# Kernel optimization log

Measured on AMD Instinct MI355X. Metric: run time of the kernel, lower is better.

## Reference

```python
import jax, jax.numpy as jnp
import numpy as np

EPS = 1e-12  # torch F.normalize default eps


def setup_inputs() -> dict:
    key = jax.random.key(0)
    k1, k2, k3, k4 = jax.random.split(key, 4)
    B, M, D = 4, 8192, 512
    N, P = 128, 1
    x = jax.random.normal(k1, (B, M, D), dtype=jnp.float32)
    phi = jax.random.normal(k2, (D, N, P), dtype=jnp.float32) * (1.0 / D ** 0.5)
    scale = jnp.ones((1,), dtype=jnp.float32)
    W = jax.random.normal(k3, (N, D, D), dtype=jnp.float32) * (1.0 / D ** 0.5)
    b = jax.random.normal(k4, (N, D), dtype=jnp.float32) * 0.01
    return {"x": x, "phi": phi, "scale": scale, "W": W, "b": b}


def _l2norm(v, axis):
    return v / jnp.maximum(jnp.linalg.norm(v, axis=axis, keepdims=True), EPS)


def reference(x, phi, scale, W, b):
    # normalize tokens along feature dim, phi along dim axis, scale phi
    xn = _l2norm(x, axis=2)                      # [B,M,D]
    phin = scale * _l2norm(phi, axis=0)          # [D,N,P]
    logits = jnp.einsum('bmd,dnp->bmnp', xn, phin)
    B, M, N, P = logits.shape
    d = jax.nn.softmax(logits, axis=1)           # dispatch weights (over tokens)
    c = jax.nn.softmax(logits.reshape(B, M, N * P), axis=-1).reshape(B, M, N, P)  # combine (over slots)
    xs = jnp.einsum('bmd,bmnp->bnpd', xn, d)     # slot inputs [B,N,P,D]
    # per-expert Linear, batched over experts (grouped GEMM)
    ys = jnp.einsum('bnpd,nde->bnpe', xs, W) + b[None, :, None, :]
    y = jnp.einsum('bnpd,bmnp->bmd', ys, c)
    return y
```

## Files before the change

### kernel.cpp

```cpp
#include <hip/hip_runtime.h>
#include <math.h>

#define B_ 4
#define M_ 8192
#define D_ 512
#define N_ 128
#define TOK (B_ * M_)
#define MC_ 64
#define MLEN (M_ / MC_)

#define OFF_RN 0
#define OFF_CS (OFF_RN + TOK)
#define OFF_XS (OFF_CS + 512)
#define OFF_YS (OFF_XS + B_ * N_ * D_)
#define OFF_PBT (OFF_YS + B_ * N_ * D_)
#define OFF_YST (OFF_PBT + N_ * D_ / 2)
#define OFF_E (OFF_YST + B_ * D_ * N_ / 2)
#define OFF_XP (OFF_E + (size_t)TOK * N_)

typedef __attribute__((ext_vector_type(8))) short s16x8;
typedef __attribute__((ext_vector_type(4))) float f32x4;

__device__ inline short f2bf(float f) {
    union { float f; unsigned u; } v;
    v.f = f;
    unsigned r = v.u + 0x7fffu + ((v.u >> 16) & 1u);
    return (short)(r >> 16);
}

__global__ __launch_bounds__(128) void k_phinorm(const float* __restrict__ phi,
                                                 const float* __restrict__ scale,
                                                 short* __restrict__ pbt) {
    __shared__ float sred[128];
    int n = blockIdx.x, tid = threadIdx.x;
    float ss = 0.f;
    for (int d = tid; d < D_; d += 128) {
        float v = phi[d * N_ + n];
        ss += v * v;
    }
    sred[tid] = ss;
    __syncthreads();
    for (int s = 64; s > 0; s >>= 1) {
        if (tid < s) sred[tid] += sred[tid + s];
        __syncthreads();
    }
    float sc = scale[0] / fmaxf(sqrtf(sred[0]), 1e-12f);
    for (int d = tid; d < D_; d += 128) pbt[n * D_ + d] = f2bf(phi[d * N_ + n] * sc);
}

__global__ __launch_bounds__(256) void k_rn(const float* __restrict__ x,
                                            float* __restrict__ rn) {
    int token = blockIdx.x * 4 + (threadIdx.x >> 6);
    int lane = threadIdx.x & 63;
    const float4* x4 = (const float4*)x;
    float4 a = x4[(size_t)token * 128 + lane];
    float4 c = x4[(size_t)token * 128 + 64 + lane];
    float ss = a.x * a.x + a.y * a.y + a.z * a.z + a.w * a.w +
               c.x * c.x + c.y * c.y + c.z * c.z + c.w * c.w;
#pragma unroll
    for (int off = 32; off > 0; off >>= 1) ss += __shfl_down(ss, off, 64);
    if (lane == 0) rn[token] = 1.0f / fmaxf(sqrtf(ss), 1e-12f);
}

__global__ __launch_bounds__(512) void k_logits(const float* __restrict__ x,
                                                const short* __restrict__ pbt,
                                                const float* __restrict__ rn,
                                                float* __restrict__ E,
                                                float* __restrict__ colsum) {
    __shared__ short As[128 * 40];
    __shared__ short Bs[128 * 40];
    int t = threadIdx.x;
    int r0 = blockIdx.x * 128;
    int sm = t >> 2;
    int kq = (t & 3) * 8;
    float rnv = rn[r0 + sm];
    const float* xrow = &x[(size_t)(r0 + sm) * D_ + kq];
    const short* brow = &pbt[sm * D_ + kq];
    int wid = t >> 6, lane = t & 63;
    int quad = lane >> 4, l15 = lane & 15;
    int mw = (wid >> 1) * 32, nw = (wid & 1) * 64;
    f32x4 acc[2][4] = {};

    for (int k0 = 0; k0 < D_; k0 += 32) {
        float4 a0 = *(const float4*)&xrow[k0];
        float4 a1 = *(const float4*)&xrow[k0 + 4];
        s16x8 bv = *(const s16x8*)&brow[k0];
        short4 w0 = {f2bf(a0.x * rnv), f2bf(a0.y * rnv), f2bf(a0.z * rnv), f2bf(a0.w * rnv)};
        short4 w1 = {f2bf(a1.x * rnv), f2bf(a1.y * rnv), f2bf(a1.z * rnv), f2bf(a1.w * rnv)};
        *(short4*)&As[sm * 40 + kq] = w0;
        *(short4*)&As[sm * 40 + kq + 4] = w1;
        *(s16x8*)&Bs[sm * 40 + kq] = bv;
        __syncthreads();
        s16x8 af[2], bf[4];
#pragma unroll
        for (int i = 0; i < 2; i++)
            af[i] = *(const s16x8*)&As[(mw + i * 16 + l15) * 40 + quad * 8];
#pragma unroll
        for (int j = 0; j < 4; j++)
            bf[j] = *(const s16x8*)&Bs[(nw + j * 16 + l15) * 40 + quad * 8];
#pragma unroll
        for (int i = 0; i < 2; i++)
#pragma unroll
            for (int j = 0; j < 4; j++)
                acc[i][j] = __builtin_amdgcn_mfma_f32_16x16x32_bf16(af[i], bf[j], acc[i][j], 0, 0, 0);
        __syncthreads();
    }
    int bb = r0 >> 13;
#pragma unroll
    for (int j = 0; j < 4; j++) {
        int n = nw + j * 16 + l15;
        float cs = 0.f;
#pragma unroll
        for (int i = 0; i < 2; i++) {
            int mb = r0 + mw + i * 16 + quad * 4;
            f32x4 v = acc[i][j];
            float e0 = __expf(v[0]), e1 = __expf(v[1]), e2 = __expf(v[2]), e3 = __expf(v[3]);
            cs += e0 + e1 + e2 + e3;
            E[(size_t)(mb + 0) * N_ + n] = e0;
            E[(size_t)(mb + 1) * N_ + n] = e1;
            E[(size_t)(mb + 2) * N_ + n] = e2;
            E[(size_t)(mb + 3) * N_ + n] = e3;
        }
        cs += __shfl_xor(cs, 16, 64);
        cs += __shfl_xor(cs, 32, 64);
        if (lane < 16) atomicAdd(&colsum[bb * N_ + n], cs);
    }
}

__global__ __launch_bounds__(256) void k_xs(const float* __restrict__ x,
                                            const float* __restrict__ E,
                                            const float* __restrict__ rn,
                                            float* __restrict__ part) {
    __shared__ float Et[16][128];
    __shared__ float xt[16][128];
    int tid = threadIdx.x, bi = blockIdx.x;
    int dt = bi & 3, mc = (bi >> 2) & 63, b = bi >> 8;
    int d0 = dt * 128;
    int rbase = b * M_ + mc * MLEN;
    int ty = tid >> 4, tx = tid & 15;
    float acc[8][8];
#pragma unroll
    for (int i = 0; i < 8; i++)
#pragma unroll
        for (int j = 0; j < 8; j++) acc[i][j] = 0.f;

    for (int ms = 0; ms < MLEN; ms += 16) {
        int rb = rbase + ms;
        {
            int lmm = tid >> 4, lc4 = (tid & 15) * 4;
            float rr = rn[rb + lmm];
            const float* Er = &E[(size_t)(rb + lmm) * N_];
            const float* xr = &x[(size_t)(rb + lmm) * D_ + d0];
            float4 v0 = *(const float4*)&Er[lc4];
            float4 v1 = *(const float4*)&Er[64 + lc4];
            v0.x *= rr; v0.y *= rr; v0.z *= rr; v0.w *= rr;
            v1.x *= rr; v1.y *= rr; v1.z *= rr; v1.w *= rr;
            *(float4*)&Et[lmm][lc4] = v0;
            *(float4*)&Et[lmm][64 + lc4] = v1;
            *(float4*)&xt[lmm][lc4] = *(const float4*)&xr[lc4];
            *(float4*)&xt[lmm][64 + lc4] = *(const float4*)&xr[64 + lc4];
        }
        __syncthreads();
#pragma unroll
        for (int kk = 0; kk < 16; kk++) {
            float4 a0 = *(float4*)&Et[kk][ty * 4];
            float4 a1 = *(float4*)&Et[kk][64 + ty * 4];
            float4 b0 = *(float4*)&xt[kk][tx * 4];
            float4 b1 = *(float4*)&xt[kk][64 + tx * 4];
            float a8[8] = {a0.x, a0.y, a0.z, a0.w, a1.x, a1.y, a1.z, a1.w};
            float b8[8] = {b0.x, b0.y, b0.z, b0.w, b1.x, b1.y, b1.z, b1.w};
#pragma unroll
            for (int i = 0; i < 8; i++)
#pragma unroll
                for (int j = 0; j < 8; j++) acc[i][j] += a8[i] * b8[j];
        }
        __syncthreads();
    }
#pragma unroll
    for (int i = 0; i < 8; i++) {
        int n = (i < 4) ? (ty * 4 + i) : (64 + ty * 4 + (i - 4));
        size_t base = (((size_t)mc * B_ + b) * N_ + n) * D_ + d0;
        float4 v0 = {acc[i][0], acc[i][1], acc[i][2], acc[i][3]};
        float4 v1 = {acc[i][4], acc[i][5], acc[i][6], acc[i][7]};
        *(float4*)&part[base + tx * 4] = v0;
        *(float4*)&part[base + 64 + tx * 4] = v1;
    }
}

__global__ __launch_bounds__(256) void k_xsum(const float* __restrict__ part,
                                              const float* __restrict__ colsum,
                                              float* __restrict__ xs) {
    int bi = blockIdx.x;
    int tid = threadIdx.x;
    float inv = 1.0f / colsum[bi];
    size_t base = (size_t)bi * D_ + tid * 2;
    float sx = 0.f, sy = 0.f;
#pragma unroll 8
    for (int mc = 0; mc < MC_; mc++) {
        float2 v = *(const float2*)&part[(size_t)mc * (B_ * N_ * D_) + base];
        sx += v.x;
        sy += v.y;
    }
    float2 o = {sx * inv, sy * inv};
    *(float2*)&xs[base] = o;
}

__global__ __launch_bounds__(256) void k_ys(const float* __restrict__ xs,
                                            const float* __restrict__ W,
                                            const float* __restrict__ bias,
                                            float* __restrict__ ys) {
    __shared__ float xsn[B_][D_];
    int bi = blockIdx.x;
    int n = bi >> 2, eq = bi & 3;
    int tid = threadIdx.x;
    {
        int lb = tid >> 6, ld = (tid & 63) * 4;
        *(float4*)&xsn[lb][ld] = *(const float4*)&xs[((size_t)lb * N_ + n) * D_ + ld];
        *(float4*)&xsn[lb][256 + ld] =
            *(const float4*)&xs[((size_t)lb * N_ + n) * D_ + 256 + ld];
    }
    __syncthreads();
    int b = tid >> 6;
    int e = eq * 128 + (tid & 63) * 2;
    const float* Wn = W + (size_t)n * D_ * D_ + e;
    float a0 = 0.f, a1 = 0.f;
#pragma unroll 8
    for (int d = 0; d < D_; d++) {
        float2 w = *(const float2*)&Wn[(size_t)d * D_];
        float xv = xsn[b][d];
        a0 += xv * w.x;
        a1 += xv * w.y;
    }
    float2 bv = *(const float2*)&bias[n * D_ + e];
    float2 o = {a0 + bv.x, a1 + bv.y};
    *(float2*)&ys[((size_t)b * N_ + n) * D_ + e] = o;
}

__global__ __launch_bounds__(256) void k_yst(const float* __restrict__ ys,
                                             short* __restrict__ ysT) {
    __shared__ float tile[32][33];
    int bi = blockIdx.x;
    int nt = bi & 3, dt = (bi >> 2) & 15, b = bi >> 6;
    int n0 = nt * 32, d0 = dt * 32;
    int t = threadIdx.x;
    int r = t >> 3, c = (t & 7) * 4;
    float4 v = *(const float4*)&ys[((size_t)b * N_ + n0 + r) * D_ + d0 + c];
    tile[r][c] = v.x; tile[r][c + 1] = v.y; tile[r][c + 2] = v.z; tile[r][c + 3] = v.w;
    __syncthreads();
    short4 o = {f2bf(tile[c][r]), f2bf(tile[c + 1][r]), f2bf(tile[c + 2][r]),
                f2bf(tile[c + 3][r])};
    *(short4*)&ysT[((size_t)b * D_ + d0 + r) * N_ + n0 + c] = o;
}

__global__ __launch_bounds__(256) void k_combine(const float* __restrict__ E,
                                                 const short* __restrict__ ysT,
                                                 float* __restrict__ y) {
    __shared__ short As[128 * 40];
    __shared__ short Bs[128 * 40];
    __shared__ float rsA[2][128];
    __shared__ float rsinv[128];
    int t = threadIdx.x, bi = blockIdx.x;
    int dt = bi & 3, mt = bi >> 2;
    int r0 = mt * 128, d0 = dt * 128;
    int bb = r0 >> 13;
    int sm = t >> 1, nh = (t & 1) * 16;
    const float* erow = &E[(size_t)(r0 + sm) * N_ + nh];
    const short* yrow = &ysT[((size_t)bb * D_ + d0 + sm) * N_ + nh];
    int wid = t >> 6, lane = t & 63;
    int quad = lane >> 4, l15 = lane & 15;
    int mw = (wid >> 1) * 64, dw = (wid & 1) * 64;
    f32x4 acc[4][4] = {};
    float rsp = 0.f;

    for (int ks = 0; ks < 4; ks++) {
        int n0 = ks * 32;
        float4 e0 = *(const float4*)&erow[n0];
        float4 e1 = *(const float4*)&erow[n0 + 4];
        float4 e2 = *(const float4*)&erow[n0 + 8];
        float4 e3 = *(const float4*)&erow[n0 + 12];
        rsp += e0.x + e0.y + e0.z + e0.w + e1.x + e1.y + e1.z + e1.w +
               e2.x + e2.y + e2.z + e2.w + e3.x + e3.y + e3.z + e3.w;
        short4 w0 = {f2bf(e0.x), f2bf(e0.y), f2bf(e0.z), f2bf(e0.w)};
        short4 w1 = {f2bf(e1.x), f2bf(e1.y), f2bf(e1.z), f2bf(e1.w)};
        short4 w2 = {f2bf(e2.x), f2bf(e2.y), f2bf(e2.z), f2bf(e2.w)};
        short4 w3 = {f2bf(e3.x), f2bf(e3.y), f2bf(e3.z), f2bf(e3.w)};
        *(short4*)&As[sm * 40 + nh + 0] = w0;
        *(short4*)&As[sm * 40 + nh + 4] = w1;
        *(short4*)&As[sm * 40 + nh + 8] = w2;
        *(short4*)&As[sm * 40 + nh + 12] = w3;
        *(s16x8*)&Bs[sm * 40 + nh] = *(const s16x8*)&yrow[n0];
        *(s16x8*)&Bs[sm * 40 + nh + 8] = *(const s16x8*)&yrow[n0 + 8];
        __syncthreads();
        s16x8 af[4], bf[4];
#pragma unroll
        for (int i = 0; i < 4; i++)
            af[i] = *(const s16x8*)&As[(mw + i * 16 + l15) * 40 + quad * 8];
#pragma unroll
        for (int j = 0; j < 4; j++)
            bf[j] = *(const s16x8*)&Bs[(dw + j * 16 + l15) * 40 + quad * 8];
#pragma unroll
        for (int i = 0; i < 4; i++)
#pragma unroll
            for (int j = 0; j < 4; j++)
                acc[i][j] = __builtin_amdgcn_mfma_f32_16x16x32_bf16(af[i], bf[j], acc[i][j], 0, 0, 0);
        __syncthreads();
    }
    rsA[t & 1][sm] = rsp;
    __syncthreads();
    if (t < 128) rsinv[t] = 1.0f / (rsA[0][t] + rsA[1][t]);
    __syncthreads();
#pragma unroll
    for (int i = 0; i < 4; i++) {
        int mb = mw + i * 16 + quad * 4;
        float i0 = rsinv[mb], i1 = rsinv[mb + 1], i2 = rsinv[mb + 2], i3 = rsinv[mb + 3];
#pragma unroll
        for (int j = 0; j < 4; j++) {
            int d = d0 + dw + j * 16 + l15;
            f32x4 v = acc[i][j];
            y[(size_t)(r0 + mb + 0) * D_ + d] = v[0] * i0;
            y[(size_t)(r0 + mb + 1) * D_ + d] = v[1] * i1;
            y[(size_t)(r0 + mb + 2) * D_ + d] = v[2] * i2;
            y[(size_t)(r0 + mb + 3) * D_ + d] = v[3] * i3;
        }
    }
}

extern "C" void kernel_launch(void* const* d_in, const int* in_sizes, int n_in,
                              void* d_out, int out_size, void* d_ws, size_t ws_size,
                              hipStream_t stream) {
    const float* x = (const float*)d_in[0];
    const float* phi = (const float*)d_in[1];
    const float* scale = (const float*)d_in[2];
    const float* W = (const float*)d_in[3];
    const float* bias = (const float*)d_in[4];
    float* y = (float*)d_out;
    float* ws = (float*)d_ws;

    float* rn = ws + OFF_RN;
    float* colsum = ws + OFF_CS;
    float* xs = ws + OFF_XS;
    float* ysb = ws + OFF_YS;
    short* pbt = (short*)(ws + OFF_PBT);
    short* ysT = (short*)(ws + OFF_YST);
    float* E = ws + OFF_E;
    float* part = ws + OFF_XP;

    hipMemsetAsync(colsum, 0, 512 * sizeof(float), stream);

    k_phinorm<<<N_, 128, 0, stream>>>(phi, scale, pbt);
    k_rn<<<TOK / 4, 256, 0, stream>>>(x, rn);
    k_logits<<<TOK / 128, 512, 0, stream>>>(x, pbt, rn, E, colsum);
    k_xs<<<B_ * MC_ * 4, 256, 0, stream>>>(x, E, rn, part);
    k_xsum<<<B_ * N_, 256, 0, stream>>>(part, colsum, xs);
    k_ys<<<N_ * 4, 256, 0, stream>>>(xs, W, bias, ysb);
    k_yst<<<B_ * 16 * 4, 256, 0, stream>>>(ysb, ysT);
    k_combine<<<(TOK / 128) * 4, 256, 0, stream>>>(E, ysT, y);
}
```

Baseline: 374.4 us.

## Move dispatch reduction onto bf16 MFMA with pre-transposed normalized inputs

A new prep kernel normalizes x once, writing bf16 row-major and token-transposed copies, and replaces the separate row-norm kernel. The logits kernel now reads bf16 x and additionally writes a transposed bf16 copy of exp(logits). The slot-input reduction (k_xs) becomes a bf16 MFMA GEMM over tokens instead of an FP32 scalar outer-product loop, with half as many token chunks. The ys kernel writes the transposed bf16 output directly, which removes the separate transpose kernel. This trades extra workspace traffic and reduced precision in the dispatch sum for matrix-core throughput.

Result: faster. 355.5 us (-5.1%).

```diff
diff --git a/kernel.cpp b/kernel.cpp
--- a/kernel.cpp
+++ b/kernel.cpp
@@ -6,17 +6,18 @@
 #define D_ 512
 #define N_ 128
 #define TOK (B_ * M_)
-#define MC_ 64
+#define MC_ 32
 #define MLEN (M_ / MC_)
 
-#define OFF_RN 0
-#define OFF_CS (OFF_RN + TOK)
+#define OFF_CS 0
 #define OFF_XS (OFF_CS + 512)
-#define OFF_YS (OFF_XS + B_ * N_ * D_)
-#define OFF_PBT (OFF_YS + B_ * N_ * D_)
-#define OFF_YST (OFF_PBT + N_ * D_ / 2)
-#define OFF_E (OFF_YST + B_ * D_ * N_ / 2)
-#define OFF_XP (OFF_E + (size_t)TOK * N_)
+#define OFF_PBT (OFF_XS + B_ * N_ * D_)
+#define OFF_E (OFF_PBT + N_ * D_ / 2)
+#define OFF_EWT (OFF_E + (size_t)TOK * N_)
+#define OFF_XB (OFF_EWT + (size_t)N_ * TOK / 2)
+#define OFF_XBT (OFF_XB + (size_t)TOK * D_ / 2)
+#define OFF_YST (OFF_XBT + (size_t)D_ * TOK / 2)
+#define OFF_XP (OFF_YST + B_ * D_ * N_ / 2)
 
 typedef __attribute__((ext_vector_type(8))) short s16x8;
 typedef __attribute__((ext_vector_type(4))) float f32x4;
@@ -48,33 +49,69 @@
     for (int d = tid; d < D_; d += 128) pbt[n * D_ + d] = f2bf(phi[d * N_ + n] * sc);
 }
 
-__global__ __launch_bounds__(256) void k_rn(const float* __restrict__ x,
-                                            float* __restrict__ rn) {
-    int token = blockIdx.x * 4 + (threadIdx.x >> 6);
-    int lane = threadIdx.x & 63;
-    const float4* x4 = (const float4*)x;
-    float4 a = x4[(size_t)token * 128 + lane];
-    float4 c = x4[(size_t)token * 128 + 64 + lane];
-    float ss = a.x * a.x + a.y * a.y + a.z * a.z + a.w * a.w +
-               c.x * c.x + c.y * c.y + c.z * c.z + c.w * c.w;
-#pragma unroll
-    for (int off = 32; off > 0; off >>= 1) ss += __shfl_down(ss, off, 64);
-    if (lane == 0) rn[token] = 1.0f / fmaxf(sqrtf(ss), 1e-12f);
-}
-
-__global__ __launch_bounds__(512) void k_logits(const float* __restrict__ x,
+__global__ __launch_bounds__(256) void k_prep(const float* __restrict__ x,
+                                              short* __restrict__ xb,
+                                              short* __restrict__ xbt) {
+    __shared__ short T[512 * 40];
+    __shared__ float sred[32][8];
+    __shared__ float srn[32];
+    int t = threadIdx.x;
+    int m0 = blockIdx.x * 32;
+    int row = t >> 3, o8 = t & 7;
+    const float4* xr = (const float4*)&x[(size_t)(m0 + row) * D_ + o8 * 64];
+    float4 v[16];
+    float ss = 0.f;
+#pragma unroll
+    for (int i = 0; i < 16; i++) {
+        v[i] = xr[i];
+        ss += v[i].x * v[i].x + v[i].y * v[i].y + v[i].z * v[i].z + v[i].w * v[i].w;
+    }
+    sred[row][o8] = ss;
+    __syncthreads();
+    if (t < 32) {
+        float s = sred[t][0] + sred[t][1] + sred[t][2] + sred[t][3] +
+                  sred[t][4] + sred[t][5] + sred[t][6] + sred[t][7];
+        srn[t] = 1.0f / fmaxf(sqrtf(s), 1e-12f);
+    }
+    __syncthreads();
+    float rv = srn[row];
+    short* xrow = &xb[(size_t)(m0 + row) * D_ + o8 * 64];
+    int slot = (row + 8 * (o8 & 3)) & 31;
+    int dbase = o8 * 64;
+#pragma unroll
+    for (int i = 0; i < 16; i++) {
+        short4 w = {f2bf(v[i].x * rv), f2bf(v[i].y * rv), f2bf(v[i].z * rv), f2bf(v[i].w * rv)};
+        *(short4*)&xrow[i * 4] = w;
+        int d = dbase + i * 4;
+        T[(d + 0) * 40 + slot] = w.x;
+        T[(d + 1) * 40 + slot] = w.y;
+        T[(d + 2) * 40 + slot] = w.z;
+        T[(d + 3) * 40 + slot] = w.w;
+    }
+    __syncthreads();
+#pragma unroll
+    for (int p = 0; p < 8; p++) {
+        int d = p * 64 + (t >> 2);
+        int g = t & 3;
+        int sgrp = (g + ((d >> 6) & 3)) & 3;
+        s16x8 val = *(const s16x8*)&T[d * 40 + sgrp * 8];
+        *(s16x8*)&xbt[(size_t)d * TOK + m0 + g * 8] = val;
+    }
+}
+
+__global__ __launch_bounds__(512) void k_logits(const short* __restrict__ xb,
                                                 const short* __restrict__ pbt,
-                                                const float* __restrict__ rn,
                                                 float* __restrict__ E,
+                                                short* __restrict__ ewt,
                                                 float* __restrict__ colsum) {
-    __shared__ short As[128 * 40];
-    __shared__ short Bs[128 * 40];
+    __shared__ short smem[2 * 128 * 40];
+    short* As = smem;
+    short* Bs = smem + 128 * 40;
     int t = threadIdx.x;
     int r0 = blockIdx.x * 128;
     int sm = t >> 2;
     int kq = (t & 3) * 8;
-    float rnv = rn[r0 + sm];
-    const float* xrow = &x[(size_t)(r0 + sm) * D_ + kq];
+    const short* xrow = &xb[(size_t)(r0 + sm) * D_ + kq];
     const short* brow = &pbt[sm * D_ + kq];
     int wid = t >> 6, lane = t & 63;
     int quad = lane >> 4, l15 = lane & 15;
@@ -82,13 +119,9 @@
     f32x4 acc[2][4] = {};
 
     for (int k0 = 0; k0 < D_; k0 += 32) {
-        float4 a0 = *(const float4*)&xrow[k0];
-        float4 a1 = *(const float4*)&xrow[k0 + 4];
+        s16x8 av = *(const s16x8*)&xrow[k0];
         s16x8 bv = *(const s16x8*)&brow[k0];
-        short4 w0 = {f2bf(a0.x * rnv), f2bf(a0.y * rnv), f2bf(a0.z * rnv), f2bf(a0.w * rnv)};
-        short4 w1 = {f2bf(a1.x * rnv), f2bf(a1.y * rnv), f2bf(a1.z * rnv), f2bf(a1.w * rnv)};
-        *(short4*)&As[sm * 40 + kq] = w0;
-        *(short4*)&As[sm * 40 + kq + 4] = w1;
+        *(s16x8*)&As[sm * 40 + kq] = av;
         *(s16x8*)&Bs[sm * 40 + kq] = bv;
         __syncthreads();
         s16x8 af[2], bf[4];
@@ -106,6 +139,7 @@
         __syncthreads();
     }
     int bb = r0 >> 13;
+    short4 ebf[2][4];
 #pragma unroll
     for (int j = 0; j < 4; j++) {
         int n = nw + j * 16 + l15;
@@ -113,77 +147,101 @@
 #pragma unroll
         for (int i = 0; i < 2; i++) {
             int mb = r0 + mw + i * 16 + quad * 4;
-            f32x4 v = acc[i][j];
-            float e0 = __expf(v[0]), e1 = __expf(v[1]), e2 = __expf(v[2]), e3 = __expf(v[3]);
+            f32x4 vv = acc[i][j];
+            float e0 = __expf(vv[0]), e1 = __expf(vv[1]), e2 = __expf(vv[2]), e3 = __expf(vv[3]);
             cs += e0 + e1 + e2 + e3;
             E[(size_t)(mb + 0) * N_ + n] = e0;
             E[(size_t)(mb + 1) * N_ + n] = e1;
             E[(size_t)(mb + 2) * N_ + n] = e2;
             E[(size_t)(mb + 3) * N_ + n] = e3;
+            short4 eb = {f2bf(e0), f2bf(e1), f2bf(e2), f2bf(e3)};
+            ebf[i][j] = eb;
         }
         cs += __shfl_xor(cs, 16, 64);
         cs += __shfl_xor(cs, 32, 64);
         if (lane < 16) atomicAdd(&colsum[bb * N_ + n], cs);
     }
-}
-
-__global__ __launch_bounds__(256) void k_xs(const float* __restrict__ x,
-                                            const float* __restrict__ E,
-                                            const float* __restrict__ rn,
+    short* T = smem;
+#pragma unroll
+    for (int h = 0; h < 2; h++) {
+        if ((wid & 1) == h) {
+#pragma unroll
+            for (int i = 0; i < 2; i++) {
+                int mb = mw + i * 16 + quad * 4;
+#pragma unroll
+                for (int j = 0; j < 4; j++) {
+                    int nl = j * 16 + l15;
+                    *(short4*)&T[nl * 136 + mb] = ebf[i][j];
+                }
+            }
+        }
+        __syncthreads();
+        {
+            int nl = t >> 3, c = t & 7;
+            s16x8 v0 = *(const s16x8*)&T[nl * 136 + c * 16];
+            s16x8 v1 = *(const s16x8*)&T[nl * 136 + c * 16 + 8];
+            size_t go = (size_t)(h * 64 + nl) * TOK + r0 + c * 16;
+            *(s16x8*)&ewt[go] = v0;
+            *(s16x8*)&ewt[go + 8] = v1;
+        }
+        __syncthreads();
+    }
+}
+
+__global__ __launch_bounds__(256) void k_xs(const short* __restrict__ ewt,
+                                            const short* __restrict__ xbt,
                                             float* __restrict__ part) {
-    __shared__ float Et[16][128];
-    __shared__ float xt[16][128];
-    int tid = threadIdx.x, bi = blockIdx.x;
-    int dt = bi & 3, mc = (bi >> 2) & 63, b = bi >> 8;
+    __shared__ short An[128 * 40];
+    __shared__ short Bd[128 * 40];
+    int t = threadIdx.x, bi = blockIdx.x;
+    int dt = bi & 3, mc = (bi >> 2) & 31, b = bi >> 7;
     int d0 = dt * 128;
-    int rbase = b * M_ + mc * MLEN;
-    int ty = tid >> 4, tx = tid & 15;
-    float acc[8][8];
-#pragma unroll
-    for (int i = 0; i < 8; i++)
-#pragma unroll
-        for (int j = 0; j < 8; j++) acc[i][j] = 0.f;
-
-    for (int ms = 0; ms < MLEN; ms += 16) {
-        int rb = rbase + ms;
-        {
-            int lmm = tid >> 4, lc4 = (tid & 15) * 4;
-            float rr = rn[rb + lmm];
-            const float* Er = &E[(size_t)(rb + lmm) * N_];
-            const float* xr = &x[(size_t)(rb + lmm) * D_ + d0];
-            float4 v0 = *(const float4*)&Er[lc4];
-            float4 v1 = *(const float4*)&Er[64 + lc4];
-            v0.x *= rr; v0.y *= rr; v0.z *= rr; v0.w *= rr;
-            v1.x *= rr; v1.y *= rr; v1.z *= rr; v1.w *= rr;
-            *(float4*)&Et[lmm][lc4] = v0;
-            *(float4*)&Et[lmm][64 + lc4] = v1;
-            *(float4*)&xt[lmm][lc4] = *(const float4*)&xr[lc4];
-            *(float4*)&xt[lmm][64 + lc4] = *(const float4*)&xr[64 + lc4];
+    size_t mbase = (size_t)b * M_ + (size_t)mc * MLEN;
+    int srow = t >> 1, shalf = (t & 1) * 16;
+    const short* arow = &ewt[(size_t)srow * TOK + mbase + shalf];
+    const short* brow = &xbt[(size_t)(d0 + srow) * TOK + mbase + shalf];
+    int wid = t >> 6, lane = t & 63;
+    int quad = lane >> 4, l15 = lane & 15;
+    int nw = (wid >> 1) * 64, dw = (wid & 1) * 64;
+    f32x4 acc[4][4] = {};
+
+    for (int k0 = 0; k0 < MLEN; k0 += 32) {
+        s16x8 a0 = *(const s16x8*)&arow[k0];
+        s16x8 a1 = *(const s16x8*)&arow[k0 + 8];
+        s16x8 b0 = *(const s16x8*)&brow[k0];
+        s16x8 b1 = *(const s16x8*)&brow[k0 + 8];
+        *(s16x8*)&An[srow * 40 + shalf] = a0;
+        *(s16x8*)&An[srow * 40 + shalf + 8] = a1;
+        *(s16x8*)&Bd[srow * 40 + shalf] = b0;
+        *(s16x8*)&Bd[srow * 40 + shalf + 8] = b1;
+        __syncthreads();
+        s16x8 af[4], bf[4];
+#pragma unroll
+        for (int i = 0; i < 4; i++)
+            af[i] = *(const s16x8*)&An[(nw + i * 16 + l15) * 40 + quad * 8];
+#pragma unroll
+        for (int j = 0; j < 4; j++)
+            bf[j] = *(const s16x8*)&Bd[(dw + j * 16 + l15) * 40 + quad * 8];
+#pragma unroll
+        for (int i = 0; i < 4; i++)
+#pragma unroll
+            for (int j = 0; j < 4; j++)
+                acc[i][j] = __builtin_amdgcn_mfma_f32_16x16x32_bf16(af[i], bf[j], acc[i][j], 0, 0, 0);
+        __syncthreads();
+    }
+    size_t pbase = (((size_t)mc * B_ + b) * N_) * D_ + d0;
+#pragma unroll
+    for (int i = 0; i < 4; i++) {
+        int nb = nw + i * 16 + quad * 4;
+#pragma unroll
+        for (int j = 0; j < 4; j++) {
+            int d = dw + j * 16 + l15;
+            f32x4 vv = acc[i][j];
+            part[pbase + (size_t)(nb + 0) * D_ + d] = vv[0];
+            part[pbase + (size_t)(nb + 1) * D_ + d] = vv[1];
+            part[pbase + (size_t)(nb + 2) * D_ + d] = vv[2];
+            part[pbase + (size_t)(nb + 3) * D_ + d] = vv[3];
         }
-        __syncthreads();
-#pragma unroll
-        for (int kk = 0; kk < 16; kk++) {
-            float4 a0 = *(float4*)&Et[kk][ty * 4];
-            float4 a1 = *(float4*)&Et[kk][64 + ty * 4];
-            float4 b0 = *(float4*)&xt[kk][tx * 4];
-            float4 b1 = *(float4*)&xt[kk][64 + tx * 4];
-            float a8[8] = {a0.x, a0.y, a0.z, a0.w, a1.x, a1.y, a1.z, a1.w};
-            float b8[8] = {b0.x, b0.y, b0.z, b0.w, b1.x, b1.y, b1.z, b1.w};
-#pragma unroll
-            for (int i = 0; i < 8; i++)
-#pragma unroll
-                for (int j = 0; j < 8; j++) acc[i][j] += a8[i] * b8[j];
-        }
-        __syncthreads();
-    }
-#pragma unroll
-    for (int i = 0; i < 8; i++) {
-        int n = (i < 4) ? (ty * 4 + i) : (64 + ty * 4 + (i - 4));
-        size_t base = (((size_t)mc * B_ + b) * N_ + n) * D_ + d0;
-        float4 v0 = {acc[i][0], acc[i][1], acc[i][2], acc[i][3]};
-        float4 v1 = {acc[i][4], acc[i][5], acc[i][6], acc[i][7]};
-        *(float4*)&part[base + tx * 4] = v0;
-        *(float4*)&part[base + 64 + tx * 4] = v1;
     }
 }
 
@@ -208,7 +266,7 @@
 __global__ __launch_bounds__(256) void k_ys(const float* __restrict__ xs,
                                             const float* __restrict__ W,
                                             const float* __restrict__ bias,
-                                            float* __restrict__ ys) {
+                                            short* __restrict__ ysT) {
     __shared__ float xsn[B_][D_];
     int bi = blockIdx.x;
     int n = bi >> 2, eq = bi & 3;
@@ -232,24 +290,8 @@
         a1 += xv * w.y;
     }
     float2 bv = *(const float2*)&bias[n * D_ + e];
-    float2 o = {a0 + bv.x, a1 + bv.y};
-    *(float2*)&ys[((size_t)b * N_ + n) * D_ + e] = o;
-}
-
-__global__ __launch_bounds__(256) void k_yst(const float* __restrict__ ys,
-                                             short* __restrict__ ysT) {
-    __shared__ float tile[32][33];
-    int bi = blockIdx.x;
-    int nt = bi & 3, dt = (bi >> 2) & 15, b = bi >> 6;
-    int n0 = nt * 32, d0 = dt * 32;
-    int t = threadIdx.x;
-    int r = t >> 3, c = (t & 7) * 4;
-    float4 v = *(const float4*)&ys[((size_t)b * N_ + n0 + r) * D_ + d0 + c];
-    tile[r][c] = v.x; tile[r][c + 1] = v.y; tile[r][c + 2] = v.z; tile[r][c + 3] = v.w;
-    __syncthreads();
-    short4 o = {f2bf(tile[c][r]), f2bf(tile[c + 1][r]), f2bf(tile[c + 2][r]),
-                f2bf(tile[c + 3][r])};
-    *(short4*)&ysT[((size_t)b * D_ + d0 + r) * N_ + n0 + c] = o;
+    ysT[((size_t)b * D_ + e) * N_ + n] = f2bf(a0 + bv.x);
+    ysT[((size_t)b * D_ + e + 1) * N_ + n] = f2bf(a1 + bv.y);
 }
 
 __global__ __launch_bounds__(256) void k_combine(const float* __restrict__ E,
@@ -336,23 +378,23 @@
     float* y = (float*)d_out;
     float* ws = (float*)d_ws;
 
-    float* rn = ws + OFF_RN;
     float* colsum = ws + OFF_CS;
     float* xs = ws + OFF_XS;
-    float* ysb = ws + OFF_YS;
     short* pbt = (short*)(ws + OFF_PBT);
+    float* E = ws + OFF_E;
+    short* ewt = (short*)(ws + OFF_EWT);
+    short* xb = (short*)(ws + OFF_XB);
+    short* xbt = (short*)(ws + OFF_XBT);
     short* ysT = (short*)(ws + OFF_YST);
-    float* E = ws + OFF_E;
     float* part = ws + OFF_XP;
 
     hipMemsetAsync(colsum, 0, 512 * sizeof(float), stream);
 
     k_phinorm<<<N_, 128, 0, stream>>>(phi, scale, pbt);
-    k_rn<<<TOK / 4, 256, 0, stream>>>(x, rn);
-    k_logits<<<TOK / 128, 512, 0, stream>>>(x, pbt, rn, E, colsum);
-    k_xs<<<B_ * MC_ * 4, 256, 0, stream>>>(x, E, rn, part);
+    k_prep<<<TOK / 32, 256, 0, stream>>>(x, xb, xbt);
+    k_logits<<<TOK / 128, 512, 0, stream>>>(xb, pbt, E, ewt, colsum);
+    k_xs<<<B_ * MC_ * 4, 256, 0, stream>>>(ewt, xbt, part);
     k_xsum<<<B_ * N_, 256, 0, stream>>>(part, colsum, xs);
-    k_ys<<<N_ * 4, 256, 0, stream>>>(xs, W, bias, ysb);
-    k_yst<<<B_ * 16 * 4, 256, 0, stream>>>(ysb, ysT);
+    k_ys<<<N_ * 4, 256, 0, stream>>>(xs, W, bias, ysT);
     k_combine<<<(TOK / 128) * 4, 256, 0, stream>>>(E, ysT, y);
 }
```
